# Performance work log

Measured on AMD Instinct MI355X. Metric: run time of the kernel, lower is better.

Reference implementation:

```python
import jax, jax.numpy as jnp
import numpy as np

N_NODES = 50000
N_EDGES = 800000
NODE_DIM = 64
EDGE_DIM = 32
OUT_FEATS = 64


def setup_inputs() -> dict:
    key = jax.random.key(0)
    k1, k2, k3, k4, k5, k6, k7 = jax.random.split(key, 7)
    node_features = jax.random.normal(k1, (N_NODES, NODE_DIM), dtype=jnp.float32)
    edge_features = jax.random.normal(k2, (N_EDGES, EDGE_DIM), dtype=jnp.float32)
    src = jax.random.randint(k3, (N_EDGES,), 0, N_NODES, dtype=jnp.int32)
    dst = jax.random.randint(k4, (N_EDGES,), 0, N_NODES, dtype=jnp.int32)
    in_dim = 2 * NODE_DIM + EDGE_DIM  # concat([e_ft, h_src, h_dst])
    w_group = jax.random.normal(k5, (in_dim,), dtype=jnp.float32) * 0.05
    w_srcattn = jax.random.normal(k6, (NODE_DIM + EDGE_DIM,), dtype=jnp.float32) * 0.05
    w_lin = jax.random.normal(k7, (in_dim, OUT_FEATS), dtype=jnp.float32) * 0.05
    return {"node_features": node_features, "edge_features": edge_features,
            "src": src, "dst": dst,
            "w_group": w_group, "w_srcattn": w_srcattn, "w_lin": w_lin}


def _segment_softmax(scores, seg, num_segments):
    # numerically-stable softmax of per-edge scalar scores within each segment
    m = jax.ops.segment_max(scores, seg, num_segments=num_segments)
    e = jnp.exp(scores - m[seg])
    s = jax.ops.segment_sum(e, seg, num_segments=num_segments)
    return e / s[seg]


def reference(node_features, edge_features, src, dst, w_group, w_srcattn, w_lin):
    h = node_features              # [N, node_dim]
    e_ft = edge_features           # [E, edge_dim]
    h_src = h[src]                 # [E, node_dim]
    h_dst = h[dst]                 # [E, node_dim]

    # --- group_apply_edges(group_by='src'): edge attention over out-edges of each src ---
    z2 = jnp.concatenate([e_ft, h_src, h_dst], axis=1)      # [E, edge_dim + 2*node_dim]
    a = z2 @ w_group                                        # [E]
    gamma = _segment_softmax(a, src, N_NODES)               # softmax over edges sharing src
    e_weighted = gamma[:, None] * e_ft                      # [E, edge_dim]

    # --- gnn_msg: msg = concat([h_src, e_weighted]) ---
    msg = jnp.concatenate([h_src, e_weighted], axis=1)      # [E, node_dim + edge_dim]

    # --- gnn_reduce: attention softmax over mailbox (edges sharing dst), weighted sum ---
    s = msg @ w_srcattn                                     # [E]
    alpha = _segment_softmax(s, dst, N_NODES)
    accum = jax.ops.segment_sum(alpha[:, None] * msg, dst, num_segments=N_NODES)  # [N, node_dim+edge_dim]

    # --- node_update: linear(concat([h, accum])) + relu ---
    h_cat = jnp.concatenate([h, accum], axis=1)             # [N, 2*node_dim + edge_dim]
    out = jax.nn.relu(h_cat @ w_lin)                        # [N, out_feats]
    return out
```

## Files before the change

### kernel.cpp

```cpp
#include <hip/hip_runtime.h>

#define NN 50000
#define NE 800000
#define NHB 3125

__global__ __launch_bounds__(256) void k_pre(
    const float* __restrict__ h, const int* __restrict__ dst,
    const float* __restrict__ wg, const float* __restrict__ wa,
    int* __restrict__ cnt, int* __restrict__ rank,
    float* __restrict__ p1, float* __restrict__ pd, float* __restrict__ dpf)
{
    int tid = threadIdx.x;
    if (blockIdx.x < NHB) {
        int e = blockIdx.x * 256 + tid;
        if (e < NE) rank[e] = atomicAdd(&cnt[dst[e]], 1);
        return;
    }
    __shared__ float4 ls[16], ld[16], lt[16];
    if (tid < 16)      ls[tid]      = ((const float4*)wg)[8 + tid];
    else if (tid < 32) ld[tid - 16] = ((const float4*)wg)[8 + tid];
    else if (tid < 48) lt[tid - 32] = ((const float4*)wa)[tid - 32];
    __syncthreads();
    int n = (blockIdx.x - NHB) * 16 + (tid >> 4);
    if (n >= NN) return;
    int l16 = tid & 15;
    float4 v = ((const float4*)(h + (size_t)n * 64))[l16];
    float4 w1 = ls[l16], w2 = ld[l16], w3 = lt[l16];
    float s1 = v.x*w1.x + v.y*w1.y + v.z*w1.z + v.w*w1.w;
    float s2 = v.x*w2.x + v.y*w2.y + v.z*w2.z + v.w*w2.w;
    float s3 = v.x*w3.x + v.y*w3.y + v.z*w3.z + v.w*w3.w;
    #pragma unroll
    for (int m = 8; m; m >>= 1) {
        s1 += __shfl_xor(s1, m);
        s2 += __shfl_xor(s2, m);
        s3 += __shfl_xor(s3, m);
    }
    if (l16 == 0) { p1[n] = s1; pd[n] = s2; dpf[2 * n + 1] = s3; }
}

__global__ __launch_bounds__(256) void k_assign(
    const int* __restrict__ cnt, int* __restrict__ off, int* __restrict__ gtotal)
{
    int n = blockIdx.x * 256 + threadIdx.x;
    int lane = threadIdx.x & 63;
    int c = (n < NN) ? cnt[n] : 0;
    int pre = c;
    #pragma unroll
    for (int d = 1; d < 64; d <<= 1) {
        int v = __shfl_up(pre, d);
        if (lane >= d) pre += v;
    }
    int base = 0;
    if (lane == 63) base = atomicAdd(gtotal, pre);
    base = __shfl(base, 63);
    if (n < NN) off[n] = base + pre - c;
}

__global__ __launch_bounds__(256) void k_edge(
    const float* __restrict__ ef, const int* __restrict__ src,
    const int* __restrict__ dst, const int* __restrict__ rank,
    const float* __restrict__ wg, const float* __restrict__ wa,
    const float* __restrict__ p1, const float* __restrict__ pd,
    float* __restrict__ dpf, const int* __restrict__ off,
    int4* __restrict__ recA)
{
    __shared__ float4 lwe[8], lae[8];
    int tid = threadIdx.x;
    if (tid < 8)       lwe[tid]     = ((const float4*)wg)[tid];
    else if (tid < 16) lae[tid - 8] = ((const float4*)wa)[tid - 8 + 16];
    __syncthreads();
    int e = blockIdx.x * 256 + tid;
    if (e >= NE) return;
    int s = src[e], d = dst[e], rk = rank[e];
    const float4* e4 = (const float4*)(ef + (size_t)e * 32);
    float a = 0.f, u = 0.f;
    #pragma unroll
    for (int q = 0; q < 8; ++q) {
        float4 v = e4[q], w = lwe[q], w2 = lae[q];
        a += v.x*w.x  + v.y*w.y  + v.z*w.z  + v.w*w.w;
        u += v.x*w2.x + v.y*w2.y + v.z*w2.z + v.w*w2.w;
    }
    a += p1[s] + pd[d];
    float eav = __expf(a);
    atomicAdd(&dpf[2 * s], eav);
    int pos = off[d] + rk;
    recA[pos] = make_int4(s, e, __float_as_int(eav), __float_as_int(u));
}

__global__ __launch_bounds__(256) void k_reduce(
    const float* __restrict__ h, const float* __restrict__ ef,
    const int* __restrict__ cnt, const int* __restrict__ off,
    const float2* __restrict__ dp, const int4* __restrict__ recA,
    float* __restrict__ accum)
{
    int n = blockIdx.x * 4 + (threadIdx.x >> 6);
    if (n >= NN) return;
    int lane = threadIdx.x & 63;
    bool up = lane >= 32;
    int l5 = lane & 31;
    int deg = cnt[n], base = off[n];
    float acch = 0.f, acce = 0.f, den = 0.f;
    int j = 0;
    for (; j + 4 <= deg; j += 4) {
        int4 r0 = recA[base+j+0], r1 = recA[base+j+1];
        int4 r2 = recA[base+j+2], r3 = recA[base+j+3];
        float2 d0 = dp[r0.x], d1 = dp[r1.x], d2 = dp[r2.x], d3 = dp[r3.x];
        float h0 = h[(size_t)r0.x*64+lane], h1 = h[(size_t)r1.x*64+lane];
        float h2 = h[(size_t)r2.x*64+lane], h3 = h[(size_t)r3.x*64+lane];
        int eA = up ? r1.y : r0.y, eB = up ? r3.y : r2.y;
        float efA = ef[(size_t)eA*32 + l5];
        float efB = ef[(size_t)eB*32 + l5];
        float g0 = __int_as_float(r0.z)/d0.x, g1 = __int_as_float(r1.z)/d1.x;
        float g2 = __int_as_float(r2.z)/d2.x, g3 = __int_as_float(r3.z)/d3.x;
        float s0 = __expf(d0.y + g0*__int_as_float(r0.w));
        float s1 = __expf(d1.y + g1*__int_as_float(r1.w));
        float s2 = __expf(d2.y + g2*__int_as_float(r2.w));
        float s3 = __expf(d3.y + g3*__int_as_float(r3.w));
        den  += s0 + s1 + s2 + s3;
        acch += s0*h0 + s1*h1 + s2*h2 + s3*h3;
        float wA = up ? s1*g1 : s0*g0;
        float wB = up ? s3*g3 : s2*g2;
        acce += wA*efA + wB*efB;
    }
    for (; j < deg; ++j) {
        int4 r = recA[base+j];
        float2 dt = dp[r.x];
        float g = __int_as_float(r.z)/dt.x;
        float s = __expf(dt.y + g*__int_as_float(r.w));
        den += s;
        acch += s * h[(size_t)r.x*64+lane];
        if (!up) acce += s * g * ef[(size_t)r.y*32 + l5];
    }
    acce += __shfl_xor(acce, 32);
    float inv = (deg > 0) ? 1.f/den : 0.f;
    accum[(size_t)n*96 + lane] = acch * inv;
    if (!up) accum[(size_t)n*96 + 64 + lane] = acce * inv;
}

__global__ __launch_bounds__(256) void k_node_update(
    const float* __restrict__ h, const float* __restrict__ accum,
    const float* __restrict__ wl_g, float* __restrict__ out)
{
    __shared__ float wl[160 * 64];
    for (int i = threadIdx.x; i < 160 * 64; i += 256) wl[i] = wl_g[i];
    __syncthreads();
    int o = threadIdx.x & 63;
    int nsub = threadIdx.x >> 6;
    for (int n = blockIdx.x * 4 + nsub; n < NN; n += gridDim.x * 4) {
        const float4* h4 = (const float4*)(h + (size_t)n * 64);
        const float4* a4 = (const float4*)(accum + (size_t)n * 96);
        float acc = 0.f;
        #pragma unroll
        for (int q = 0; q < 16; ++q) {
            float4 v = h4[q];
            int k = q * 4;
            acc += v.x * wl[(k + 0) * 64 + o] + v.y * wl[(k + 1) * 64 + o]
                 + v.z * wl[(k + 2) * 64 + o] + v.w * wl[(k + 3) * 64 + o];
        }
        #pragma unroll
        for (int q = 0; q < 24; ++q) {
            float4 v = a4[q];
            int k = 64 + q * 4;
            acc += v.x * wl[(k + 0) * 64 + o] + v.y * wl[(k + 1) * 64 + o]
                 + v.z * wl[(k + 2) * 64 + o] + v.w * wl[(k + 3) * 64 + o];
        }
        out[(size_t)n * 64 + o] = fmaxf(acc, 0.f);
    }
}

extern "C" void kernel_launch(void* const* d_in, const int* in_sizes, int n_in,
                              void* d_out, int out_size, void* d_ws, size_t ws_size,
                              hipStream_t stream)
{
    const float* h   = (const float*)d_in[0];
    const float* ef  = (const float*)d_in[1];
    const int*   src = (const int*)d_in[2];
    const int*   dst = (const int*)d_in[3];
    const float* wg  = (const float*)d_in[4];
    const float* wa  = (const float*)d_in[5];
    const float* wl  = (const float*)d_in[6];
    float* out = (float*)d_out;

    float* ws = (float*)d_ws;
    float*  dpf    = ws;
    int*    cnt    = (int*)(ws + 2 * NN);
    int*    gtotal = (int*)(ws + 3 * NN);
    int*    off    = (int*)(ws + 3 * NN + 16);
    float*  p1     = ws + 4 * NN + 16;
    float*  pd     = ws + 5 * NN + 16;
    int4*   recA   = (int4*)(ws + 6 * NN + 16);
    int*    rank   = (int*)(ws + 6 * NN + 16 + 4 * NE);
    float*  accum  = ws + 6 * NN + 16 + 4 * NE;

    hipMemsetAsync(d_ws, 0, (size_t)(3 * NN + 16) * sizeof(float), stream);

    k_pre<<<2 * NHB, 256, 0, stream>>>(h, dst, wg, wa, cnt, rank, p1, pd, dpf);
    k_assign<<<(NN + 255) / 256, 256, 0, stream>>>(cnt, off, gtotal);
    k_edge<<<NHB, 256, 0, stream>>>(ef, src, dst, rank, wg, wa, p1, pd, dpf,
                                    off, recA);
    k_reduce<<<(NN + 3) / 4, 256, 0, stream>>>(h, ef, cnt, off, (const float2*)dpf,
                                               recA, accum);
    k_node_update<<<1024, 256, 0, stream>>>(h, accum, wl, out);
}
```

Baseline: 403.3 us.

## Use bf16 MFMA for node update linear layer with register-resident weights

Rewrites the final node-update GEMM to use 16x16x32 bf16 MFMA instructions instead of scalar FMAs over an LDS-staged weight matrix. Each wave keeps the whole converted weight matrix in registers and processes 16-node tiles, converting activations to bf16 on the fly. The grid shrinks to 256 blocks. The aim is to cut the ALU and LDS cost of the dense layer, at the price of bf16 rounding error and heavy register use.

```diff
diff --git a/kernel.cpp b/kernel.cpp
--- a/kernel.cpp
+++ b/kernel.cpp
@@ -3,6 +3,16 @@
 #define NN 50000
 #define NE 800000
 #define NHB 3125
+#define NTILES 3125
+
+typedef __attribute__((ext_vector_type(8))) short bf16x8;
+typedef __attribute__((ext_vector_type(4))) float f32x4;
+
+static __device__ __forceinline__ short f2bf(float f) {
+    unsigned int u = __float_as_uint(f);
+    u += 0x7FFFu + ((u >> 16) & 1u);
+    return (short)(u >> 16);
+}
 
 __global__ __launch_bounds__(256) void k_pre(
     const float* __restrict__ h, const int* __restrict__ dst,
@@ -141,30 +151,57 @@
     const float* __restrict__ h, const float* __restrict__ accum,
     const float* __restrict__ wl_g, float* __restrict__ out)
 {
-    __shared__ float wl[160 * 64];
-    for (int i = threadIdx.x; i < 160 * 64; i += 256) wl[i] = wl_g[i];
-    __syncthreads();
-    int o = threadIdx.x & 63;
-    int nsub = threadIdx.x >> 6;
-    for (int n = blockIdx.x * 4 + nsub; n < NN; n += gridDim.x * 4) {
-        const float4* h4 = (const float4*)(h + (size_t)n * 64);
-        const float4* a4 = (const float4*)(accum + (size_t)n * 96);
-        float acc = 0.f;
-        #pragma unroll
-        for (int q = 0; q < 16; ++q) {
-            float4 v = h4[q];
-            int k = q * 4;
-            acc += v.x * wl[(k + 0) * 64 + o] + v.y * wl[(k + 1) * 64 + o]
-                 + v.z * wl[(k + 2) * 64 + o] + v.w * wl[(k + 3) * 64 + o];
+    int lane = threadIdx.x & 63;
+    int col  = lane & 15;
+    int quad = lane >> 4;
+    int wid  = blockIdx.x * 4 + (threadIdx.x >> 6);
+    int nwaves = gridDim.x * 4;
+
+    bf16x8 bfr[5][4];
+    #pragma unroll
+    for (int kc = 0; kc < 5; ++kc)
+        #pragma unroll
+        for (int nt = 0; nt < 4; ++nt) {
+            #pragma unroll
+            for (int j = 0; j < 8; ++j) {
+                int k = kc * 32 + quad * 8 + j;
+                bfr[kc][nt][j] = f2bf(wl_g[k * 64 + nt * 16 + col]);
+            }
         }
-        #pragma unroll
-        for (int q = 0; q < 24; ++q) {
-            float4 v = a4[q];
-            int k = 64 + q * 4;
-            acc += v.x * wl[(k + 0) * 64 + o] + v.y * wl[(k + 1) * 64 + o]
-                 + v.z * wl[(k + 2) * 64 + o] + v.w * wl[(k + 3) * 64 + o];
+
+    for (int tile = wid; tile < NTILES; tile += nwaves) {
+        int n = tile * 16 + col;
+        f32x4 acc[4];
+        #pragma unroll
+        for (int nt = 0; nt < 4; ++nt) acc[nt] = (f32x4){0.f, 0.f, 0.f, 0.f};
+
+        #pragma unroll
+        for (int kc = 0; kc < 5; ++kc) {
+            int kbase = kc * 32 + quad * 8;
+            const float* p = (kbase < 64)
+                ? (h     + (size_t)n * 64 + kbase)
+                : (accum + (size_t)n * 96 + (kbase - 64));
+            float4 va = *(const float4*)p;
+            float4 vb = *(const float4*)(p + 4);
+            bf16x8 af;
+            af[0] = f2bf(va.x); af[1] = f2bf(va.y);
+            af[2] = f2bf(va.z); af[3] = f2bf(va.w);
+            af[4] = f2bf(vb.x); af[5] = f2bf(vb.y);
+            af[6] = f2bf(vb.z); af[7] = f2bf(vb.w);
+            #pragma unroll
+            for (int nt = 0; nt < 4; ++nt)
+                acc[nt] = __builtin_amdgcn_mfma_f32_16x16x32_bf16(
+                    af, bfr[kc][nt], acc[nt], 0, 0, 0);
         }
-        out[(size_t)n * 64 + o] = fmaxf(acc, 0.f);
+
+        #pragma unroll
+        for (int nt = 0; nt < 4; ++nt) {
+            #pragma unroll
+            for (int r = 0; r < 4; ++r) {
+                int node = tile * 16 + quad * 4 + r;
+                out[(size_t)node * 64 + nt * 16 + col] = fmaxf(acc[nt][r], 0.f);
+            }
+        }
     }
 }
 
@@ -200,5 +237,5 @@
                                     off, recA);
     k_reduce<<<(NN + 3) / 4, 256, 0, stream>>>(h, ef, cnt, off, (const float2*)dpf,
                                                recA, accum);
-    k_node_update<<<1024, 256, 0, stream>>>(h, accum, wl, out);
-}
+    k_node_update<<<256, 256, 0, stream>>>(h, accum, wl, out);
+}
```

Result: faster. 336.6 us (-16.5%).
